# Kernel optimization log

Hardware: AMD Instinct MI355X
Metric: run time of the kernel (lower is better)

The kernel has to match this reference:

```python
import jax, jax.numpy as jnp
import numpy as np


def setup_inputs() -> dict:
    key = jax.random.key(0)
    ks = jax.random.split(key, 4)
    B, S, D, H, E = 2, 2048, 1024, 4096, 8
    scale_in = 1.0 / np.sqrt(D)
    scale_h = 1.0 / np.sqrt(H)
    return {
        "x": jax.random.normal(ks[0], (B, S, D), dtype=jnp.float32),
        "Wr": jax.random.normal(ks[1], (E, D), dtype=jnp.float32) * scale_in,
        "br": jnp.zeros((E,), dtype=jnp.float32),
        "W1": jax.random.normal(ks[2], (E, H, D), dtype=jnp.float32) * scale_in,
        "b1": jnp.zeros((E, H), dtype=jnp.float32),
        "W2": jax.random.normal(ks[3], (E, D, H), dtype=jnp.float32) * scale_h,
        "b2": jnp.zeros((E, D), dtype=jnp.float32),
        "top_k": 2,
    }


def reference(x, Wr, br, W1, b1, W2, b2, top_k):
    B, S, D = x.shape
    E = Wr.shape[0]
    x_flat = x.reshape(-1, D)                                   # [N, D]
    # Router: top-k logits, softmax over the selected k values only
    logits = x_flat @ Wr.T + br                                 # [N, E]
    top_vals, top_idx = jax.lax.top_k(logits, top_k)            # [N, k]
    gates = jax.nn.softmax(top_vals, axis=-1)                   # [N, k]
    # Per-expert combine weight: gate_e[n, e] = sum_k gates[n, k] * 1[top_idx[n,k]==e]
    gate_e = jnp.einsum("nk,nke->ne", gates,
                        jax.nn.one_hot(top_idx, E, dtype=x.dtype))  # [N, E]
    # Dense all-expert MLP (grouped GEMM), then masked combine. Same math as
    # the per-expert gather/scatter loop: unselected experts get zero gate.
    h = jax.nn.relu(jnp.einsum("nd,ehd->neh", x_flat, W1) + b1)     # [N, E, H]
    y = jnp.einsum("neh,edh->ned", h, W2) + b2                      # [N, E, D]
    out = jnp.einsum("ned,ne->nd", y, gate_e)                       # [N, D]
    return out.reshape(B, S, D)
```

## Files before the change

kernel.cpp:

```cpp
#include <hip/hip_runtime.h>
#include <hip/hip_bf16.h>
#include <stdint.h>

#define N_TOK 4096
#define D_ 1024
#define H_ 4096
#define E_ 8
#define NSLOT (N_TOK*2)
#define BM 128
#define BN 128
#define BK 32
#define MAXT 72

typedef __attribute__((ext_vector_type(8))) short short8;
typedef __attribute__((ext_vector_type(4))) float floatx4;
typedef unsigned int u32;

__device__ __forceinline__ unsigned short f2bf(float f){
    union { float f; unsigned int u; } c; c.f = f;
    unsigned int u = c.u;
    unsigned int r = (u + 0x7fffu + ((u >> 16) & 1u)) >> 16;
    return (unsigned short)r;
}

__device__ __forceinline__ void async16(const void* g, void* l){
    __builtin_amdgcn_global_load_lds(
        (const __attribute__((address_space(1))) u32*)g,
        (__attribute__((address_space(3))) u32*)l, 16, 0, 0);
}

__global__ __launch_bounds__(256) void cvt_kernel(
    const float* __restrict__ src, unsigned short* __restrict__ dst, int n4)
{
    int stride = gridDim.x * 256;
    for (int i = blockIdx.x * 256 + threadIdx.x; i < n4; i += stride){
        float4 v = ((const float4*)src)[i];
        ushort4 o; o.x=f2bf(v.x); o.y=f2bf(v.y); o.z=f2bf(v.z); o.w=f2bf(v.w);
        ((ushort4*)dst)[i] = o;
    }
}

__global__ __launch_bounds__(256) void router_kernel(
    const float* __restrict__ x, const float* __restrict__ Wr,
    const float* __restrict__ br, int* __restrict__ topIdx,
    float* __restrict__ topGate)
{
    int n = blockIdx.x * 4 + (threadIdx.x >> 6);
    int lane = threadIdx.x & 63;
    const float4* xp = (const float4*)(x + (size_t)n * D_);
    float acc[E_];
#pragma unroll
    for (int e = 0; e < E_; e++) acc[e] = 0.f;
#pragma unroll
    for (int j = 0; j < 4; j++){
        int idx = j * 64 + lane;
        float4 xv = xp[idx];
#pragma unroll
        for (int e = 0; e < E_; e++){
            float4 wv = ((const float4*)(Wr + (size_t)e * D_))[idx];
            acc[e] += xv.x*wv.x + xv.y*wv.y + xv.z*wv.z + xv.w*wv.w;
        }
    }
#pragma unroll
    for (int e = 0; e < E_; e++){
        float v = acc[e];
        for (int off = 32; off > 0; off >>= 1) v += __shfl_xor(v, off, 64);
        acc[e] = v;
    }
    if (lane == 0){
        float best = -1e30f, second = -1e30f; int bi = 0, si = 0;
#pragma unroll
        for (int e = 0; e < E_; e++){
            float v = acc[e] + br[e];
            if (v > best){ second = best; si = bi; best = v; bi = e; }
            else if (v > second){ second = v; si = e; }
        }
        float e1 = __expf(second - best);
        float denom = 1.f + e1;
        topIdx[n*2+0] = bi;  topIdx[n*2+1] = si;
        topGate[n*2+0] = 1.f/denom;  topGate[n*2+1] = e1/denom;
    }
}

__global__ __launch_bounds__(256) void hist_kernel(
    const int* __restrict__ topIdx, int* __restrict__ hdr)
{
    __shared__ int c[E_];
    int t = threadIdx.x;
    if (t < E_) c[t] = 0;
    __syncthreads();
    int e = topIdx[blockIdx.x * 256 + t];
    atomicAdd(&c[e], 1);
    __syncthreads();
    if (t < E_) hdr[256 + blockIdx.x * E_ + t] = c[t];
}

__global__ __launch_bounds__(64) void scan2_kernel(int* __restrict__ hdr)
{
    __shared__ int cnt[32 * E_];
    __shared__ int tot[E_];
    __shared__ int offs[E_ + 1];
    int t = threadIdx.x;
    for (int i = t; i < 32 * E_; i += 64) cnt[i] = hdr[256 + i];
    __syncthreads();
    if (t < E_){
        int s = 0;
        for (int b = 0; b < 32; b++) s += cnt[b * E_ + t];
        tot[t] = s;
    }
    __syncthreads();
    if (t == 0){
        int o = 0;
        for (int e = 0; e < E_; e++){ offs[e] = o; o += tot[e]; }
        offs[E_] = o;
    }
    __syncthreads();
    if (t < E_ + 1) hdr[16 + t] = offs[t];
    if (t < E_){
        int run = offs[t];
        for (int b = 0; b < 32; b++){ hdr[512 + b * E_ + t] = run; run += cnt[b * E_ + t]; }
    }
    if (t == 0){
        int tn = 0;
        for (int e = 0; e < E_; e++){
            int nt = (tot[e] + BM - 1) >> 7;
            for (int i = 0; i < nt; i++){ hdr[32 + tn] = e; hdr[112 + tn] = offs[e] + (i << 7); tn++; }
        }
        for (; tn < MAXT; tn++){ hdr[32 + tn] = -1; hdr[112 + tn] = 0; }
    }
}

__global__ __launch_bounds__(256) void pos_kernel(
    const int* __restrict__ topIdx, const float* __restrict__ topGate,
    const int* __restrict__ hdr, int* __restrict__ posOf,
    int* __restrict__ rowTok, float* __restrict__ rowGate)
{
    __shared__ int c[E_];
    int t = threadIdx.x;
    if (t < E_) c[t] = 0;
    __syncthreads();
    int slot = blockIdx.x * 256 + t;
    int e = topIdx[slot];
    int r = atomicAdd(&c[e], 1);
    int pos = hdr[512 + blockIdx.x * E_ + e] + r;
    posOf[slot] = pos;
    rowTok[pos] = slot >> 1;
    rowGate[pos] = topGate[slot];
}

__global__ __launch_bounds__(256) void copy_kernel(
    const float* __restrict__ x, const int* __restrict__ posOf,
    unsigned short* __restrict__ xg)
{
    int slot = blockIdx.x * 4 + (threadIdx.x >> 6);
    int lane = threadIdx.x & 63;
    int n = slot >> 1;
    int pos = posOf[slot];
    const float4* xp = (const float4*)(x + (size_t)n * D_);
    ushort4* op = (ushort4*)(xg + (size_t)pos * D_);
#pragma unroll
    for (int j = 0; j < 4; j++){
        float4 v = xp[j * 64 + lane];
        ushort4 o; o.x=f2bf(v.x); o.y=f2bf(v.y); o.z=f2bf(v.z); o.w=f2bf(v.w);
        op[j * 64 + lane] = o;
    }
}

template<int MODE, bool BF16B>
__global__ __launch_bounds__(256) void moe_gemm(
    const unsigned short* __restrict__ A, int Ktot,
    const void* __restrict__ Wbase, size_t wStride,
    const float* __restrict__ biasBase, int biasStride,
    const int* __restrict__ hdr,
    const int* __restrict__ rowTok, const float* __restrict__ rowGate,
    unsigned short* __restrict__ hout, float* __restrict__ out)
{
    int gid = blockIdx.y * gridDim.x + blockIdx.x;
    int per = gridDim.x * 8;
    int g = gid / per, rr = gid % per;
    int by = g * 8 + (rr & 7);
    int bx = rr >> 3;

    int e = hdr[32 + bx];
    if (e < 0) return;
    int rowBase = hdr[112 + bx];
    int validRows = hdr[16 + e + 1] - rowBase;

    int kChunk = Ktot / gridDim.z;
    int kStart = blockIdx.z * kChunk;

    __shared__ __align__(16) unsigned short As[2][BM * BK];
    __shared__ __align__(16) unsigned short BsH[BF16B ? 2 * BN * BK : 1];
    __shared__ __align__(16) float BsF[BF16B ? 1 : BN * BK];

    const float* biasE = biasBase + (size_t)e * biasStride + by * BN;

    const int tid  = threadIdx.x;
    const int lane = tid & 63, wave = tid >> 6;
    const int wm = wave & 1, wn = wave >> 1;
    const int l16 = lane & 15, quad = lane >> 4;

    floatx4 acc[4][4];
#pragma unroll
    for (int mi = 0; mi < 4; mi++)
#pragma unroll
        for (int ni = 0; ni < 4; ni++)
            acc[mi][ni] = (floatx4){0.f,0.f,0.f,0.f};

    if (BF16B){
        const unsigned short* Wexp = (const unsigned short*)Wbase
            + (size_t)e * wStride + (size_t)(by * BN) * Ktot;

        size_t aOff[2], bOff[2];
        int    lOff[2];
#pragma unroll
        for (int i = 0; i < 2; i++){
            int s = i * 256 + tid;
            int r = s >> 2, gst = s & 3;
            int gsrc = gst ^ ((r >> 1) & 3);
            int ar = rowBase + r;
            ar = ar < (NSLOT - 1) ? ar : (NSLOT - 1);
            aOff[i] = (size_t)ar * Ktot + gsrc * 8;
            bOff[i] = (size_t)r  * Ktot + gsrc * 8;
            lOff[i] = s * 16;
        }

#pragma unroll
        for (int i = 0; i < 2; i++){
            async16(A    + aOff[i] + kStart, (char*)As[0]  + lOff[i]);
            async16(Wexp + bOff[i] + kStart, (char*)BsH    + lOff[i]);
        }

        int nIter = kChunk / BK;
        for (int it = 0; it < nIter; it++){
            __syncthreads();
            int p = it & 1;
            if (it + 1 < nIter){
                int kn = kStart + (it + 1) * BK;
#pragma unroll
                for (int i = 0; i < 2; i++){
                    async16(A    + aOff[i] + kn, (char*)As[p ^ 1] + lOff[i]);
                    async16(Wexp + bOff[i] + kn, (char*)BsH + (p ^ 1) * (BN * BK * 2) + lOff[i]);
                }
            }
            short8 af[4], bfr[4];
#pragma unroll
            for (int mi = 0; mi < 4; mi++){
                int r = wm*64 + mi*16 + l16;
                int gq = quad ^ ((r >> 1) & 3);
                af[mi] = *(const short8*)(As[p] + r * BK + gq * 8);
            }
#pragma unroll
            for (int ni = 0; ni < 4; ni++){
                int n = wn*64 + ni*16 + l16;
                int gq = quad ^ ((n >> 1) & 3);
                bfr[ni] = *(const short8*)(BsH + p * (BN * BK) + n * BK + gq * 8);
            }
#pragma unroll
            for (int mi = 0; mi < 4; mi++)
#pragma unroll
                for (int ni = 0; ni < 4; ni++)
                    acc[mi][ni] = __builtin_amdgcn_mfma_f32_16x16x32_bf16(
                        af[mi], bfr[ni], acc[mi][ni], 0, 0, 0);
        }
    } else {
        const float* Wexp = (const float*)Wbase
            + (size_t)e * wStride + (size_t)(by * BN) * Ktot;
        int aS[2], aRow[2], aCol[2];
#pragma unroll
        for (int i = 0; i < 2; i++){
            int s = i * 256 + tid;
            aS[i] = s;
            int r = rowBase + (s >> 2);
            aRow[i] = r < (NSLOT - 1) ? r : (NSLOT - 1);
            aCol[i] = (s & 3) * 8;
        }
        int bS[4], bRow[4], bCol[4];
#pragma unroll
        for (int i = 0; i < 4; i++){
            int s = i * 256 + tid;
            bS[i] = s;
            int r = s >> 3, c = s & 7;
            bRow[i] = r;
            bCol[i] = (c ^ (r & 7)) * 4;
        }
        for (int k0 = kStart; k0 < kStart + kChunk; k0 += BK){
#pragma unroll
            for (int i = 0; i < 2; i++)
                async16(A + (size_t)aRow[i] * Ktot + k0 + aCol[i], (char*)As[0] + aS[i] * 16);
#pragma unroll
            for (int i = 0; i < 4; i++)
                async16(Wexp + (size_t)bRow[i] * Ktot + k0 + bCol[i], (char*)BsF + bS[i] * 16);
            __syncthreads();
            short8 af[4], bfr[4];
#pragma unroll
            for (int mi = 0; mi < 4; mi++)
                af[mi] = *(const short8*)(As[0] + (wm*64 + mi*16 + l16) * BK + quad * 8);
#pragma unroll
            for (int ni = 0; ni < 4; ni++){
                int n = wn*64 + ni*16 + l16;
                int g0 = (2*quad)     ^ (n & 7);
                int g1 = (2*quad + 1) ^ (n & 7);
                float4 u0 = *(const float4*)(BsF + n * BK + g0 * 4);
                float4 u1 = *(const float4*)(BsF + n * BK + g1 * 4);
                union { short8 s; __hip_bfloat162 h[4]; } u;
                u.h[0] = __float22bfloat162_rn(make_float2(u0.x, u0.y));
                u.h[1] = __float22bfloat162_rn(make_float2(u0.z, u0.w));
                u.h[2] = __float22bfloat162_rn(make_float2(u1.x, u1.y));
                u.h[3] = __float22bfloat162_rn(make_float2(u1.z, u1.w));
                bfr[ni] = u.s;
            }
#pragma unroll
            for (int mi = 0; mi < 4; mi++)
#pragma unroll
                for (int ni = 0; ni < 4; ni++)
                    acc[mi][ni] = __builtin_amdgcn_mfma_f32_16x16x32_bf16(
                        af[mi], bfr[ni], acc[mi][ni], 0, 0, 0);
            __syncthreads();
        }
    }

    bool addB = (MODE == 1) || (blockIdx.z == 0);
#pragma unroll
    for (int mi = 0; mi < 4; mi++){
#pragma unroll
        for (int r = 0; r < 4; r++){
            int rl = wm*64 + mi*16 + quad*4 + r;
            if (rl >= validRows) continue;
            int grow = rowBase + rl;
            int   tok  = 0;
            float gate = 0.f;
            if (MODE == 2){ tok = rowTok[grow]; gate = rowGate[grow]; }
#pragma unroll
            for (int ni = 0; ni < 4; ni++){
                int lcol = wn*64 + ni*16 + l16;
                int gcol = by * BN + lcol;
                float v = acc[mi][ni][r] + (addB ? biasE[lcol] : 0.f);
                if (MODE == 1){
                    v = v > 0.f ? v : 0.f;
                    hout[(size_t)grow * H_ + gcol] = f2bf(v);
                } else {
                    atomicAdd(out + (size_t)tok * D_ + gcol, gate * v);
                }
            }
        }
    }
}

extern "C" void kernel_launch(void* const* d_in, const int* in_sizes, int n_in,
                              void* d_out, int out_size, void* d_ws, size_t ws_size,
                              hipStream_t stream)
{
    (void)in_sizes; (void)n_in;
    const float* x  = (const float*)d_in[0];
    const float* Wr = (const float*)d_in[1];
    const float* br = (const float*)d_in[2];
    const float* W1 = (const float*)d_in[3];
    const float* b1 = (const float*)d_in[4];
    const float* W2 = (const float*)d_in[5];
    const float* b2 = (const float*)d_in[6];
    float* out = (float*)d_out;

    char* ws = (char*)d_ws;
    int*   hdr     = (int*)ws;
    int*   topIdx  = (int*)  (ws + 4096);
    float* topGate = (float*)(ws + 36864);
    int*   posOf   = (int*)  (ws + 69632);
    int*   rowTok  = (int*)  (ws + 102400);
    float* rowGate = (float*)(ws + 135168);
    unsigned short* xg   = (unsigned short*)(ws + 262144);
    unsigned short* hbuf = (unsigned short*)(ws + 17039360);
    unsigned short* w1b  = (unsigned short*)(ws + 84148224);
    unsigned short* w2b  = (unsigned short*)(ws + 151257088);
    const bool full = ws_size >= 218365952ull;

    hipMemsetAsync(d_out, 0, (size_t)out_size * sizeof(float), stream);

    router_kernel<<<N_TOK/4, 256, 0, stream>>>(x, Wr, br, topIdx, topGate);
    hist_kernel<<<32, 256, 0, stream>>>(topIdx, hdr);
    scan2_kernel<<<1, 64, 0, stream>>>(hdr);
    pos_kernel<<<32, 256, 0, stream>>>(topIdx, topGate, hdr, posOf, rowTok, rowGate);
    copy_kernel<<<NSLOT/4, 256, 0, stream>>>(x, posOf, xg);

    if (full){
        cvt_kernel<<<2048, 256, 0, stream>>>(W1, w1b, (E_*H_*D_)/4);
        cvt_kernel<<<2048, 256, 0, stream>>>(W2, w2b, (E_*D_*H_)/4);
        moe_gemm<1,true><<<dim3(MAXT, H_/BN, 1), 256, 0, stream>>>(
            xg, D_, w1b, (size_t)H_ * D_, b1, H_, hdr, rowTok, rowGate, hbuf, nullptr);
        moe_gemm<2,true><<<dim3(MAXT, D_/BN, 2), 256, 0, stream>>>(
            hbuf, H_, w2b, (size_t)D_ * H_, b2, D_, hdr, rowTok, rowGate, nullptr, out);
    } else {
        moe_gemm<1,false><<<dim3(MAXT, H_/BN, 1), 256, 0, stream>>>(
            xg, D_, W1, (size_t)H_ * D_, b1, H_, hdr, rowTok, rowGate, hbuf, nullptr);
        moe_gemm<2,false><<<dim3(MAXT, D_/BN, 2), 256, 0, stream>>>(
            hbuf, H_, W2, (size_t)D_ * H_, b2, D_, hdr, rowTok, rowGate, nullptr, out);
    }
}
```

Before: 641.5 us.

## Add 256x256-tile 4-stage pipelined grouped GEMM with XCD-aware block remap

Adds a new MoE grouped GEMM kernel with 512 threads, 256x256 tiles, and a 4-deep LDS ring filled by async global-to-LDS loads. Loads are interleaved with MFMA phases under explicit waitcnt, barriers and setprio. Block IDs are remapped so that neighbouring tiles share an XCD, and the second GEMM's split-K grows from 2 to 4. The router scan now also emits a 256-row tile table. The aim is to raise MFMA utilisation and data reuse. The cost is heavier register and LDS use, more padding waste per expert on the larger tiles, and more atomic adds in the second GEMM.

```diff
diff --git a/kernel.cpp b/kernel.cpp
--- a/kernel.cpp
+++ b/kernel.cpp
@@ -11,6 +11,10 @@
 #define BN 128
 #define BK 32
 #define MAXT 72
+#define BM2 256
+#define BN2 256
+#define BK2 32
+#define MAXT2 40
 
 typedef __attribute__((ext_vector_type(8))) short short8;
 typedef __attribute__((ext_vector_type(4))) float floatx4;
@@ -27,6 +31,11 @@
     __builtin_amdgcn_global_load_lds(
         (const __attribute__((address_space(1))) u32*)g,
         (__attribute__((address_space(3))) u32*)l, 16, 0, 0);
+}
+
+__device__ __forceinline__ void bar_fence(){
+    asm volatile("s_barrier" ::: "memory");
+    __builtin_amdgcn_sched_barrier(0);
 }
 
 __global__ __launch_bounds__(256) void cvt_kernel(
@@ -127,6 +136,12 @@
             for (int i = 0; i < nt; i++){ hdr[32 + tn] = e; hdr[112 + tn] = offs[e] + (i << 7); tn++; }
         }
         for (; tn < MAXT; tn++){ hdr[32 + tn] = -1; hdr[112 + tn] = 0; }
+        int t2 = 0;
+        for (int e = 0; e < E_; e++){
+            int nt = (tot[e] + BM2 - 1) >> 8;
+            for (int i = 0; i < nt; i++){ hdr[768 + t2] = e; hdr[808 + t2] = offs[e] + (i << 8); t2++; }
+        }
+        for (; t2 < MAXT2; t2++){ hdr[768 + t2] = -1; hdr[808 + t2] = 0; }
     }
 }
 
@@ -166,6 +181,162 @@
     }
 }
 
+template<int MODE>
+__global__ __launch_bounds__(512, 2) void moe_gemm2(
+    const unsigned short* __restrict__ A, int Ktot,
+    const unsigned short* __restrict__ Wbase, size_t wStride,
+    const float* __restrict__ biasBase, int biasStride,
+    const int* __restrict__ hdr,
+    const int* __restrict__ rowTok, const float* __restrict__ rowGate,
+    unsigned short* __restrict__ hout, float* __restrict__ out)
+{
+    int nwg  = gridDim.x * gridDim.y * gridDim.z;
+    int orig = (blockIdx.z * gridDim.y + blockIdx.y) * gridDim.x + blockIdx.x;
+    int xcd = orig & 7, loc = orig >> 3;
+    int q8 = nwg >> 3, r8 = nwg & 7;
+    int wgid = (xcd < r8 ? xcd * (q8 + 1) : r8 * (q8 + 1) + (xcd - r8) * q8) + loc;
+    int bx = wgid % gridDim.x;
+    int tt = wgid / gridDim.x;
+    int by = tt % gridDim.y;
+    int bz = tt / gridDim.y;
+
+    int e = hdr[768 + bx];
+    if (e < 0) return;
+    int rowBase = hdr[808 + bx];
+    int validRows = hdr[16 + e + 1] - rowBase;
+
+    int kChunk = Ktot / gridDim.z;
+    int kStart = bz * kChunk;
+    int nIter  = kChunk / BK2;
+
+    __shared__ __align__(16) unsigned short As[4][BM2 * BK2];
+    __shared__ __align__(16) unsigned short Bs[4][BN2 * BK2];
+
+    const int tid  = threadIdx.x;
+    const int lane = tid & 63, wave = tid >> 6;
+    const int wm = wave >> 2, wn = wave & 3;
+    const int l16 = lane & 15, quad = lane >> 4;
+
+    const unsigned short* Wexp = Wbase + (size_t)e * wStride + (size_t)(by * BN2) * Ktot;
+
+    u32 aOff[2], bOff[2], lOff[2];
+#pragma unroll
+    for (int i = 0; i < 2; i++){
+        int s = i * 512 + tid;
+        int rr = s >> 2, gst = s & 3;
+        int gsrc = gst ^ (rr & 3);
+        int ar = rowBase + rr; ar = ar < (NSLOT - 1) ? ar : (NSLOT - 1);
+        aOff[i] = (u32)ar * (u32)Ktot + (u32)(gsrc * 8);
+        bOff[i] = (u32)rr * (u32)Ktot + (u32)(gsrc * 8);
+        lOff[i] = (u32)(s * 16);
+    }
+
+    floatx4 acc[8][4];
+#pragma unroll
+    for (int mi = 0; mi < 8; mi++)
+#pragma unroll
+        for (int ni = 0; ni < 4; ni++)
+            acc[mi][ni] = (floatx4){0.f, 0.f, 0.f, 0.f};
+
+    const int pg    = quad ^ (l16 & 3);
+    const int aFrag = (wm * 128 + l16) * 32 + pg * 8;
+    const int bFrag = (wn * 64  + l16) * 32 + pg * 8;
+
+    auto issueA = [&](int kt){
+        u32 k0 = (u32)(kStart + kt * BK2);
+#pragma unroll
+        for (int i = 0; i < 2; i++)
+            async16(A + aOff[i] + k0, (char*)As[kt & 3] + lOff[i]);
+    };
+    auto issueB = [&](int kt){
+        u32 k0 = (u32)(kStart + kt * BK2);
+#pragma unroll
+        for (int i = 0; i < 2; i++)
+            async16(Wexp + bOff[i] + k0, (char*)Bs[kt & 3] + lOff[i]);
+    };
+
+    issueA(0); issueB(0);
+    if (1 < nIter){ issueA(1); issueB(1); }
+    if (2 < nIter){ issueA(2); issueB(2); }
+    if (nIter >= 3) asm volatile("s_waitcnt vmcnt(8)" ::: "memory");
+    else            asm volatile("s_waitcnt vmcnt(0)" ::: "memory");
+    bar_fence();
+
+    for (int kt = 0; kt < nIter; kt++){
+        const unsigned short* Ab = As[kt & 3];
+        const unsigned short* Bb = Bs[kt & 3];
+
+        short8 af[8];
+#pragma unroll
+        for (int mi = 0; mi < 8; mi++)
+            af[mi] = *(const short8*)(Ab + aFrag + mi * 512);
+        short8 bf0 = *(const short8*)(Bb + bFrag);
+        short8 bf1 = *(const short8*)(Bb + bFrag + 512);
+        if (kt + 3 < nIter) issueA(kt + 3);
+        bar_fence();
+        asm volatile("s_waitcnt lgkmcnt(0)" ::: "memory");
+        __builtin_amdgcn_sched_barrier(0);
+        __builtin_amdgcn_s_setprio(1);
+#pragma unroll
+        for (int mi = 0; mi < 8; mi++)
+            acc[mi][0] = __builtin_amdgcn_mfma_f32_16x16x32_bf16(af[mi], bf0, acc[mi][0], 0, 0, 0);
+#pragma unroll
+        for (int mi = 0; mi < 8; mi++)
+            acc[mi][1] = __builtin_amdgcn_mfma_f32_16x16x32_bf16(af[mi], bf1, acc[mi][1], 0, 0, 0);
+        __builtin_amdgcn_s_setprio(0);
+        bar_fence();
+
+        short8 bf2 = *(const short8*)(Bb + bFrag + 1024);
+        short8 bf3 = *(const short8*)(Bb + bFrag + 1536);
+        if (kt + 3 < nIter) issueB(kt + 3);
+        bar_fence();
+        asm volatile("s_waitcnt lgkmcnt(0)" ::: "memory");
+        __builtin_amdgcn_sched_barrier(0);
+        __builtin_amdgcn_s_setprio(1);
+#pragma unroll
+        for (int mi = 0; mi < 8; mi++)
+            acc[mi][2] = __builtin_amdgcn_mfma_f32_16x16x32_bf16(af[mi], bf2, acc[mi][2], 0, 0, 0);
+#pragma unroll
+        for (int mi = 0; mi < 8; mi++)
+            acc[mi][3] = __builtin_amdgcn_mfma_f32_16x16x32_bf16(af[mi], bf3, acc[mi][3], 0, 0, 0);
+        __builtin_amdgcn_s_setprio(0);
+        if (kt + 3 < nIter)       asm volatile("s_waitcnt vmcnt(8)" ::: "memory");
+        else if (kt + 3 == nIter) asm volatile("s_waitcnt vmcnt(4)" ::: "memory");
+        else if (kt + 2 == nIter) asm volatile("s_waitcnt vmcnt(0)" ::: "memory");
+        bar_fence();
+    }
+
+    bool addB = (MODE == 1) || (bz == 0);
+    const float* biasE = biasBase + (size_t)e * biasStride + by * BN2;
+    float biasv[4];
+#pragma unroll
+    for (int ni = 0; ni < 4; ni++)
+        biasv[ni] = addB ? biasE[wn * 64 + ni * 16 + l16] : 0.f;
+
+#pragma unroll
+    for (int mi = 0; mi < 8; mi++){
+#pragma unroll
+        for (int r2 = 0; r2 < 4; r2++){
+            int rl = wm * 128 + mi * 16 + quad * 4 + r2;
+            if (rl >= validRows) continue;
+            int grow = rowBase + rl;
+            int tok = 0; float gate = 0.f;
+            if (MODE == 2){ tok = rowTok[grow]; gate = rowGate[grow]; }
+#pragma unroll
+            for (int ni = 0; ni < 4; ni++){
+                int gcol = by * BN2 + wn * 64 + ni * 16 + l16;
+                float v = acc[mi][ni][r2] + biasv[ni];
+                if (MODE == 1){
+                    v = v > 0.f ? v : 0.f;
+                    hout[(size_t)grow * H_ + gcol] = f2bf(v);
+                } else {
+                    atomicAdd(out + (size_t)tok * D_ + gcol, gate * v);
+                }
+            }
+        }
+    }
+}
+
 template<int MODE, bool BF16B>
 __global__ __launch_bounds__(256) void moe_gemm(
     const unsigned short* __restrict__ A, int Ktot,
@@ -210,7 +381,6 @@
     if (BF16B){
         const unsigned short* Wexp = (const unsigned short*)Wbase
             + (size_t)e * wStride + (size_t)(by * BN) * Ktot;
-
         size_t aOff[2], bOff[2];
         int    lOff[2];
 #pragma unroll
@@ -224,13 +394,11 @@
             bOff[i] = (size_t)r  * Ktot + gsrc * 8;
             lOff[i] = s * 16;
         }
-
 #pragma unroll
         for (int i = 0; i < 2; i++){
             async16(A    + aOff[i] + kStart, (char*)As[0]  + lOff[i]);
             async16(Wexp + bOff[i] + kStart, (char*)BsH    + lOff[i]);
         }
-
         int nIter = kChunk / BK;
         for (int it = 0; it < nIter; it++){
             __syncthreads();
@@ -385,9 +553,9 @@
     if (full){
         cvt_kernel<<<2048, 256, 0, stream>>>(W1, w1b, (E_*H_*D_)/4);
         cvt_kernel<<<2048, 256, 0, stream>>>(W2, w2b, (E_*D_*H_)/4);
-        moe_gemm<1,true><<<dim3(MAXT, H_/BN, 1), 256, 0, stream>>>(
+        moe_gemm2<1><<<dim3(MAXT2, H_/BN2, 1), 512, 0, stream>>>(
             xg, D_, w1b, (size_t)H_ * D_, b1, H_, hdr, rowTok, rowGate, hbuf, nullptr);
-        moe_gemm<2,true><<<dim3(MAXT, D_/BN, 2), 256, 0, stream>>>(
+        moe_gemm2<2><<<dim3(MAXT2, D_/BN2, 4), 512, 0, stream>>>(
             hbuf, H_, w2b, (size_t)D_ * H_, b2, D_, hdr, rowTok, rowGate, nullptr, out);
     } else {
         moe_gemm<1,false><<<dim3(MAXT, H_/BN, 1), 256, 0, stream>>>(
```

New measurement: 682.6 us. 6.4% more time.

## Drop separate weight bf16 conversion; double-buffer fp32 weight tiles with in-kernel convert

Applied to the files above, without the earlier changes.

Removes the standalone fp32-to-bf16 weight conversion kernels and the bf16 GEMM path. Both expert GEMMs now stream fp32 weights directly into a double-buffered shared tile and convert to bf16 in registers before MFMA. MFMA issue priority is raised around the inner loop. This avoids writing and re-reading a converted weight copy each call, at the cost of double the LDS footprint and twice the bytes per weight tile load.

```diff
diff --git a/kernel.cpp b/kernel.cpp
--- a/kernel.cpp
+++ b/kernel.cpp
@@ -29,17 +29,6 @@
         (__attribute__((address_space(3))) u32*)l, 16, 0, 0);
 }
 
-__global__ __launch_bounds__(256) void cvt_kernel(
-    const float* __restrict__ src, unsigned short* __restrict__ dst, int n4)
-{
-    int stride = gridDim.x * 256;
-    for (int i = blockIdx.x * 256 + threadIdx.x; i < n4; i += stride){
-        float4 v = ((const float4*)src)[i];
-        ushort4 o; o.x=f2bf(v.x); o.y=f2bf(v.y); o.z=f2bf(v.z); o.w=f2bf(v.w);
-        ((ushort4*)dst)[i] = o;
-    }
-}
-
 __global__ __launch_bounds__(256) void router_kernel(
     const float* __restrict__ x, const float* __restrict__ Wr,
     const float* __restrict__ br, int* __restrict__ topIdx,
@@ -166,10 +155,10 @@
     }
 }
 
-template<int MODE, bool BF16B>
+template<int MODE>
 __global__ __launch_bounds__(256) void moe_gemm(
     const unsigned short* __restrict__ A, int Ktot,
-    const void* __restrict__ Wbase, size_t wStride,
+    const float* __restrict__ Wbase, size_t wStride,
     const float* __restrict__ biasBase, int biasStride,
     const int* __restrict__ hdr,
     const int* __restrict__ rowTok, const float* __restrict__ rowGate,
@@ -188,10 +177,10 @@
 
     int kChunk = Ktot / gridDim.z;
     int kStart = blockIdx.z * kChunk;
+    int nIter  = kChunk / BK;
 
     __shared__ __align__(16) unsigned short As[2][BM * BK];
-    __shared__ __align__(16) unsigned short BsH[BF16B ? 2 * BN * BK : 1];
-    __shared__ __align__(16) float BsF[BF16B ? 1 : BN * BK];
+    __shared__ __align__(16) float          BsF[2][BN * BK];
 
     const float* biasE = biasBase + (size_t)e * biasStride + by * BN;
 
@@ -200,6 +189,28 @@
     const int wm = wave & 1, wn = wave >> 1;
     const int l16 = lane & 15, quad = lane >> 4;
 
+    const float* Wexp = Wbase + (size_t)e * wStride + (size_t)(by * BN) * Ktot;
+
+    size_t aOff[2]; int aS[2];
+#pragma unroll
+    for (int i = 0; i < 2; i++){
+        int s = i * 256 + tid;
+        int r = s >> 2, gst = s & 3;
+        int gsrc = gst ^ ((r >> 1) & 3);
+        int ar = rowBase + r;
+        ar = ar < (NSLOT - 1) ? ar : (NSLOT - 1);
+        aOff[i] = (size_t)ar * Ktot + gsrc * 8;
+        aS[i] = s * 16;
+    }
+    size_t bOff[4]; int bS[4];
+#pragma unroll
+    for (int i = 0; i < 4; i++){
+        int s = i * 256 + tid;
+        int r = s >> 3, c = s & 7;
+        bOff[i] = (size_t)r * Ktot + (size_t)((c ^ (r & 7)) * 4);
+        bS[i] = s * 16;
+    }
+
     floatx4 acc[4][4];
 #pragma unroll
     for (int mi = 0; mi < 4; mi++)
@@ -207,117 +218,54 @@
         for (int ni = 0; ni < 4; ni++)
             acc[mi][ni] = (floatx4){0.f,0.f,0.f,0.f};
 
-    if (BF16B){
-        const unsigned short* Wexp = (const unsigned short*)Wbase
-            + (size_t)e * wStride + (size_t)(by * BN) * Ktot;
-
-        size_t aOff[2], bOff[2];
-        int    lOff[2];
-#pragma unroll
-        for (int i = 0; i < 2; i++){
-            int s = i * 256 + tid;
-            int r = s >> 2, gst = s & 3;
-            int gsrc = gst ^ ((r >> 1) & 3);
-            int ar = rowBase + r;
-            ar = ar < (NSLOT - 1) ? ar : (NSLOT - 1);
-            aOff[i] = (size_t)ar * Ktot + gsrc * 8;
-            bOff[i] = (size_t)r  * Ktot + gsrc * 8;
-            lOff[i] = s * 16;
-        }
-
-#pragma unroll
-        for (int i = 0; i < 2; i++){
-            async16(A    + aOff[i] + kStart, (char*)As[0]  + lOff[i]);
-            async16(Wexp + bOff[i] + kStart, (char*)BsH    + lOff[i]);
-        }
-
-        int nIter = kChunk / BK;
-        for (int it = 0; it < nIter; it++){
-            __syncthreads();
-            int p = it & 1;
-            if (it + 1 < nIter){
-                int kn = kStart + (it + 1) * BK;
-#pragma unroll
-                for (int i = 0; i < 2; i++){
-                    async16(A    + aOff[i] + kn, (char*)As[p ^ 1] + lOff[i]);
-                    async16(Wexp + bOff[i] + kn, (char*)BsH + (p ^ 1) * (BN * BK * 2) + lOff[i]);
-                }
-            }
-            short8 af[4], bfr[4];
-#pragma unroll
-            for (int mi = 0; mi < 4; mi++){
-                int r = wm*64 + mi*16 + l16;
-                int gq = quad ^ ((r >> 1) & 3);
-                af[mi] = *(const short8*)(As[p] + r * BK + gq * 8);
-            }
-#pragma unroll
-            for (int ni = 0; ni < 4; ni++){
-                int n = wn*64 + ni*16 + l16;
-                int gq = quad ^ ((n >> 1) & 3);
-                bfr[ni] = *(const short8*)(BsH + p * (BN * BK) + n * BK + gq * 8);
-            }
-#pragma unroll
-            for (int mi = 0; mi < 4; mi++)
-#pragma unroll
-                for (int ni = 0; ni < 4; ni++)
-                    acc[mi][ni] = __builtin_amdgcn_mfma_f32_16x16x32_bf16(
-                        af[mi], bfr[ni], acc[mi][ni], 0, 0, 0);
-        }
-    } else {
-        const float* Wexp = (const float*)Wbase
-            + (size_t)e * wStride + (size_t)(by * BN) * Ktot;
-        int aS[2], aRow[2], aCol[2];
-#pragma unroll
-        for (int i = 0; i < 2; i++){
-            int s = i * 256 + tid;
-            aS[i] = s;
-            int r = rowBase + (s >> 2);
-            aRow[i] = r < (NSLOT - 1) ? r : (NSLOT - 1);
-            aCol[i] = (s & 3) * 8;
-        }
-        int bS[4], bRow[4], bCol[4];
-#pragma unroll
-        for (int i = 0; i < 4; i++){
-            int s = i * 256 + tid;
-            bS[i] = s;
-            int r = s >> 3, c = s & 7;
-            bRow[i] = r;
-            bCol[i] = (c ^ (r & 7)) * 4;
-        }
-        for (int k0 = kStart; k0 < kStart + kChunk; k0 += BK){
+#pragma unroll
+    for (int i = 0; i < 2; i++)
+        async16(A + aOff[i] + kStart, (char*)As[0] + aS[i]);
+#pragma unroll
+    for (int i = 0; i < 4; i++)
+        async16(Wexp + bOff[i] + kStart, (char*)BsF[0] + bS[i]);
+
+    for (int it = 0; it < nIter; it++){
+        __syncthreads();
+        int p = it & 1;
+        if (it + 1 < nIter){
+            int kn = kStart + (it + 1) * BK;
 #pragma unroll
             for (int i = 0; i < 2; i++)
-                async16(A + (size_t)aRow[i] * Ktot + k0 + aCol[i], (char*)As[0] + aS[i] * 16);
+                async16(A + aOff[i] + kn, (char*)As[p ^ 1] + aS[i]);
 #pragma unroll
             for (int i = 0; i < 4; i++)
-                async16(Wexp + (size_t)bRow[i] * Ktot + k0 + bCol[i], (char*)BsF + bS[i] * 16);
-            __syncthreads();
-            short8 af[4], bfr[4];
-#pragma unroll
-            for (int mi = 0; mi < 4; mi++)
-                af[mi] = *(const short8*)(As[0] + (wm*64 + mi*16 + l16) * BK + quad * 8);
-#pragma unroll
-            for (int ni = 0; ni < 4; ni++){
-                int n = wn*64 + ni*16 + l16;
-                int g0 = (2*quad)     ^ (n & 7);
-                int g1 = (2*quad + 1) ^ (n & 7);
-                float4 u0 = *(const float4*)(BsF + n * BK + g0 * 4);
-                float4 u1 = *(const float4*)(BsF + n * BK + g1 * 4);
-                union { short8 s; __hip_bfloat162 h[4]; } u;
-                u.h[0] = __float22bfloat162_rn(make_float2(u0.x, u0.y));
-                u.h[1] = __float22bfloat162_rn(make_float2(u0.z, u0.w));
-                u.h[2] = __float22bfloat162_rn(make_float2(u1.x, u1.y));
-                u.h[3] = __float22bfloat162_rn(make_float2(u1.z, u1.w));
-                bfr[ni] = u.s;
-            }
-#pragma unroll
-            for (int mi = 0; mi < 4; mi++)
-#pragma unroll
-                for (int ni = 0; ni < 4; ni++)
-                    acc[mi][ni] = __builtin_amdgcn_mfma_f32_16x16x32_bf16(
-                        af[mi], bfr[ni], acc[mi][ni], 0, 0, 0);
-            __syncthreads();
-        }
+                async16(Wexp + bOff[i] + kn, (char*)BsF[p ^ 1] + bS[i]);
+        }
+        short8 af[4], bfr[4];
+#pragma unroll
+        for (int mi = 0; mi < 4; mi++){
+            int r = wm*64 + mi*16 + l16;
+            int gq = quad ^ ((r >> 1) & 3);
+            af[mi] = *(const short8*)(As[p] + r * BK + gq * 8);
+        }
+#pragma unroll
+        for (int ni = 0; ni < 4; ni++){
+            int n = wn*64 + ni*16 + l16;
+            int g0 = (2*quad)     ^ (n & 7);
+            int g1 = (2*quad + 1) ^ (n & 7);
+            float4 u0 = *(const float4*)(BsF[p] + n * BK + g0 * 4);
+            float4 u1 = *(const float4*)(BsF[p] + n * BK + g1 * 4);
+            union { short8 s; __hip_bfloat162 h[4]; } u;
+            u.h[0] = __float22bfloat162_rn(make_float2(u0.x, u0.y));
+            u.h[1] = __float22bfloat162_rn(make_float2(u0.z, u0.w));
+            u.h[2] = __float22bfloat162_rn(make_float2(u1.x, u1.y));
+            u.h[3] = __float22bfloat162_rn(make_float2(u1.z, u1.w));
+            bfr[ni] = u.s;
+        }
+        __builtin_amdgcn_s_setprio(1);
+#pragma unroll
+        for (int mi = 0; mi < 4; mi++)
+#pragma unroll
+            for (int ni = 0; ni < 4; ni++)
+                acc[mi][ni] = __builtin_amdgcn_mfma_f32_16x16x32_bf16(
+                    af[mi], bfr[ni], acc[mi][ni], 0, 0, 0);
+        __builtin_amdgcn_s_setprio(0);
     }
 
     bool addB = (MODE == 1) || (blockIdx.z == 0);
@@ -351,7 +299,7 @@
                               void* d_out, int out_size, void* d_ws, size_t ws_size,
                               hipStream_t stream)
 {
-    (void)in_sizes; (void)n_in;
+    (void)in_sizes; (void)n_in; (void)ws_size;
     const float* x  = (const float*)d_in[0];
     const float* Wr = (const float*)d_in[1];
     const float* br = (const float*)d_in[2];
@@ -370,9 +318,6 @@
     float* rowGate = (float*)(ws + 135168);
     unsigned short* xg   = (unsigned short*)(ws + 262144);
     unsigned short* hbuf = (unsigned short*)(ws + 17039360);
-    unsigned short* w1b  = (unsigned short*)(ws + 84148224);
-    unsigned short* w2b  = (unsigned short*)(ws + 151257088);
-    const bool full = ws_size >= 218365952ull;
 
     hipMemsetAsync(d_out, 0, (size_t)out_size * sizeof(float), stream);
 
@@ -382,17 +327,8 @@
     pos_kernel<<<32, 256, 0, stream>>>(topIdx, topGate, hdr, posOf, rowTok, rowGate);
     copy_kernel<<<NSLOT/4, 256, 0, stream>>>(x, posOf, xg);
 
-    if (full){
-        cvt_kernel<<<2048, 256, 0, stream>>>(W1, w1b, (E_*H_*D_)/4);
-        cvt_kernel<<<2048, 256, 0, stream>>>(W2, w2b, (E_*D_*H_)/4);
-        moe_gemm<1,true><<<dim3(MAXT, H_/BN, 1), 256, 0, stream>>>(
-            xg, D_, w1b, (size_t)H_ * D_, b1, H_, hdr, rowTok, rowGate, hbuf, nullptr);
-        moe_gemm<2,true><<<dim3(MAXT, D_/BN, 2), 256, 0, stream>>>(
-            hbuf, H_, w2b, (size_t)D_ * H_, b2, D_, hdr, rowTok, rowGate, nullptr, out);
-    } else {
-        moe_gemm<1,false><<<dim3(MAXT, H_/BN, 1), 256, 0, stream>>>(
-            xg, D_, W1, (size_t)H_ * D_, b1, H_, hdr, rowTok, rowGate, hbuf, nullptr);
-        moe_gemm<2,false><<<dim3(MAXT, D_/BN, 2), 256, 0, stream>>>(
-            hbuf, H_, W2, (size_t)D_ * H_, b2, D_, hdr, rowTok, rowGate, nullptr, out);
-    }
-}
+    moe_gemm<1><<<dim3(MAXT, H_/BN, 1), 256, 0, stream>>>(
+        xg, D_, W1, (size_t)H_ * D_, b1, H_, hdr, rowTok, rowGate, hbuf, nullptr);
+    moe_gemm<2><<<dim3(MAXT, D_/BN, 2), 256, 0, stream>>>(
+        hbuf, H_, W2, (size_t)D_ * H_, b2, D_, hdr, rowTok, rowGate, nullptr, out);
+}
```

Result: no change. 632.5 us (-1.4%).
